# Kernel optimization log

Hardware: AMD Instinct MI355X
Metric: run time of the kernel (lower is better)

Reference implementation:

```python
import jax, jax.numpy as jnp
import numpy as np
from jax import lax

B, D = 512, 256
C = 10  # hidden conv channels


def setup_inputs() -> dict:
    key = jax.random.key(0)
    ks = jax.random.split(key, 9)
    x = jax.random.normal(ks[0], (B, D, D), jnp.float32)
    w1 = jax.random.normal(ks[1], (C, 1, 1, 1), jnp.float32) * 0.1   # Conv2d(1,10,1)
    b1 = jax.random.normal(ks[2], (C,), jnp.float32) * 0.01
    w2 = jax.random.normal(ks[3], (1, C, 3, 3), jnp.float32) * 0.05  # Conv2d(10,1,3,1,1)
    b2 = jax.random.normal(ks[4], (1,), jnp.float32) * 0.01
    fc1_w = jax.random.normal(ks[5], (4, D * B), jnp.float32) * (1.0 / np.sqrt(D * B))
    fc1_b = jax.random.normal(ks[6], (4,), jnp.float32) * 0.01
    fc2_w = jax.random.normal(ks[7], (2, 4), jnp.float32) * 0.5
    fc2_b = jax.random.normal(ks[8], (2,), jnp.float32) * 0.01
    return {"x": x, "w1": w1, "b1": b1, "w2": w2, "b2": b2,
            "fc1_w": fc1_w, "fc1_b": fc1_b, "fc2_w": fc2_w, "fc2_b": fc2_b}


def reference(x, w1, b1, w2, b2, fc1_w, fc1_b, fc2_w, fc2_b):
    # edge-to-edge: E[b,i,j] = row_sum(i) + col_sum(j)
    rs = x.sum(axis=-1)          # [B, D]
    cs = x.sum(axis=-2)          # [B, D]
    e = (rs[:, :, None] + cs[:, None, :])[:, None]  # [B, 1, D, D]
    # Conv2d(1, C, 1) == per-pixel scale+bias over channels
    h = jax.nn.relu(e * w1.reshape(1, C, 1, 1) + b1.reshape(1, C, 1, 1))  # [B, C, D, D]
    # convSym: lower-triangular mask each channel
    h = h * jnp.tril(jnp.ones((D, D), jnp.float32))
    # Conv2d(C, 1, 3, stride=1, pad=1)
    y = lax.conv_general_dilated(h, w2, (1, 1), 'SAME',
                                 dimension_numbers=('NCHW', 'OIHW', 'NCHW'))
    y = jax.nn.relu(y + b2.reshape(1, 1, 1, 1))[:, 0]  # [B, D, D]
    # edge-to-vertex: v[b,i] = row_sum + col_sum
    v = y.sum(axis=-1) + y.sum(axis=-2)  # [B, D]
    flat = v.reshape(-1)                  # [B*D]
    hfc = jax.nn.relu(fc1_w @ flat + fc1_b)
    return fc2_w @ hfc + fc2_b            # [2]
```

## Files before the change

kernel.cpp:

```cpp
#include <hip/hip_runtime.h>

#define DD 256
#define BB 512
#define NL 2048

#define OFF_RS   0
#define OFF_CSP  131072
#define OFF_HFC  655360
#define OFF_PAR  655368
#define OFF_TABP 655376
#define OFF_LUT  655648

typedef float v2f __attribute__((ext_vector_type(2)));

__device__ __forceinline__ v2f mk2(float a, float b) { v2f r; r.x = a; r.y = b; return r; }

__device__ __forceinline__ v2f fma2(v2f a, v2f b, v2f c) {
#if __has_builtin(__builtin_elementwise_fma)
  return __builtin_elementwise_fma(a, b, c);
#else
  return mk2(fmaf(a.x, b.x, c.x), fmaf(a.y, b.y, c.y));
#endif
}

__device__ __forceinline__ float wave_red(float v) {
#pragma unroll
  for (int off = 32; off > 0; off >>= 1) v += __shfl_down(v, off, 64);
  return v;
}

__global__ __launch_bounds__(256) void sum_kernel(const float* __restrict__ x,
                                                  const float* __restrict__ w1,
                                                  const float* __restrict__ b1,
                                                  const float* __restrict__ w2,
                                                  float* __restrict__ ws) {
  const int bq = blockIdx.x;
  const int tid = threadIdx.x;
  if (bq == 2048) {
    const int t = tid;
    float w1v[10], b1v[10], bp[10];
    int rank[10];
#pragma unroll
    for (int c = 0; c < 10; ++c) { w1v[c] = w1[c]; b1v[c] = b1[c]; bp[c] = -b1v[c] / w1v[c]; }
#pragma unroll
    for (int c = 0; c < 10; ++c) {
      int r = 0;
#pragma unroll
      for (int k = 0; k < 10; ++k)
        r += (bp[k] < bp[c] || (bp[k] == bp[c] && k < c)) ? 1 : 0;
      rank[c] = r;
    }
    float lo = bp[0], hi = bp[0];
#pragma unroll
    for (int c = 1; c < 10; ++c) { lo = fminf(lo, bp[c]); hi = fmaxf(hi, bp[c]); }
    const float step = (hi - lo) / (float)(NL - 3);
    if (t == 0) {
      ws[OFF_PAR]     = (float)(NL - 3) / (hi - lo);
      ws[OFF_PAR + 1] = 1.0f - lo * ((float)(NL - 3) / (hi - lo));
    }
    if (t < 99) {
      const int s = t / 9, tt = t % 9;
      const int dr = tt / 3, kc = tt % 3;
      float A = 0.f, Bv = 0.f;
      for (int c = 0; c < 10; ++c) {
        bool act = (w1v[c] > 0.f) ? (rank[c] < s)
                 : ((w1v[c] < 0.f) ? (rank[c] >= s) : (b1v[c] > 0.f));
        if (act) { A += w1v[c] * w2[c * 9 + tt]; Bv += b1v[c] * w2[c * 9 + tt]; }
      }
      const int base = (s * 3 + kc) * 8;
      const int posA = (dr == 2) ? 4 : dr;
      const int posB = (dr == 2) ? 5 : (2 + dr);
      ws[OFF_TABP + base + posA] = A;
      ws[OFF_TABP + base + posB] = Bv;
      ws[OFF_TABP + base + 6] = 0.f;
      ws[OFF_TABP + base + 7] = 0.f;
    }
    unsigned short* lut = (unsigned short*)(ws + OFF_LUT);
    for (int k = t; k < NL; k += 256) {
      const float xx = lo + (float)(k - 1) * step;
      int s = 0;
#pragma unroll
      for (int c = 0; c < 10; ++c) s += (bp[c] < xx) ? 1 : 0;
      lut[k] = (unsigned short)(s * 96);
    }
    return;
  }
  const int b = bq >> 2;
  const int q = bq & 3;
  const int lane = tid & 63;
  const int wv = tid >> 6;
  __shared__ float rowp[64][65];
  __shared__ float csl[4][DD];
  __shared__ float segp[4][64];
  float4 cacc = make_float4(0.f, 0.f, 0.f, 0.f);
  const float4* px = (const float4*)(x + ((size_t)b << 16) + ((size_t)(q * 64 + wv * 16) << 8));
#pragma unroll
  for (int r = 0; r < 16; ++r) {
    float4 val = px[r * 64 + lane];
    cacc.x += val.x; cacc.y += val.y; cacc.z += val.z; cacc.w += val.w;
    rowp[wv * 16 + r][lane] = (val.x + val.y) + (val.z + val.w);
  }
  ((float4*)csl[wv])[lane] = cacc;
  __syncthreads();
  {
    const int row = tid & 63, seg = tid >> 6;
    const float* rp = rowp[row] + seg * 16;
    float s = 0.f;
#pragma unroll
    for (int k = 0; k < 16; ++k) s += rp[k];
    segp[seg][row] = s;
  }
  __syncthreads();
  if (tid < 64)
    ws[OFF_RS + b * DD + q * 64 + tid] =
        (segp[0][tid] + segp[1][tid]) + (segp[2][tid] + segp[3][tid]);
  ws[OFF_CSP + bq * DD + tid] =
      (csl[0][tid] + csl[1][tid]) + (csl[2][tid] + csl[3][tid]);
  if (bq == 0 && tid < 4) ws[OFF_HFC + tid] = 0.f;
}

__global__ __launch_bounds__(1024, 8) void conv_kernel(const float* __restrict__ b2p,
                                                       const float* __restrict__ fc1w,
                                                       float* __restrict__ ws) {
  const int b = blockIdx.x;
  const int tid = threadIdx.x;
  const int w = tid >> 6;
  const int lane = tid & 63;
  const int seg = w >> 2;
  const int wb = (w - seg) & 3;
  const int j = wb * 64 + lane;
  const int jmin = wb * 64;
  const int r0 = seg * 64, r1 = r0 + 64;

  __shared__ __align__(16) float tabP[264];
  __shared__ float rs_s[DD];
  __shared__ float cs_s[DD];
  __shared__ __align__(16) float wkA[DD][4];
  __shared__ unsigned short lut_s[NL];
  __shared__ float segsum_s[4][4];
  __shared__ float red_s[64];

  ((unsigned int*)lut_s)[tid] = ((const unsigned int*)(ws + OFF_LUT))[tid];
  if (tid < 256) {
    rs_s[tid] = ws[OFF_RS + b * DD + tid];
  } else if (tid < 512) {
    const int t = tid - 256;
    const float* csp = ws + OFF_CSP + (b * 4) * DD + t;
    cs_s[t] = (csp[0] + csp[DD]) + (csp[2 * DD] + csp[3 * DD]);
  } else if (tid < 768) {
    const int r = tid - 512;
#pragma unroll
    for (int k = 0; k < 4; ++k) wkA[r][k] = fc1w[k * (BB * DD) + b * DD + r];
  } else {
    const int u = tid - 768;
    if (u < 256) tabP[u] = ws[OFF_TABP + u];
  }
  if (tid < 8) tabP[256 + tid] = ws[OFF_TABP + 256 + tid];
  __syncthreads();
  if (tid < 16) {
    const int ss = tid >> 2, k = tid & 3;
    float s = 0.f;
#pragma unroll
    for (int r = 0; r < 64; ++r) s += wkA[ss * 64 + r][k];
    segsum_s[ss][k] = s;
  }
  __syncthreads();

  const float inv_step = ws[OFF_PAR];
  const float bias = ws[OFF_PAR + 1];
  const float b2v = b2p[0];
  const float yb = fmaxf(b2v, 0.f);
  const float fxmax = (float)(NL - 1);

  float csr[3], vf[3];
  csr[0] = (j >= 1) ? cs_s[j - 1] : 0.f;
  csr[1] = cs_s[j];
  csr[2] = (j < DD - 1) ? cs_s[j + 1] : 0.f;
  vf[0] = (j >= 1) ? 1.f : 0.f;
  vf[1] = 1.f;
  vf[2] = (j < DD - 1) ? 1.f : 0.f;
  v2f vf2[3];
#pragma unroll
  for (int kc = 0; kc < 3; ++kc) vf2[kc] = mk2(vf[kc], vf[kc]);

  const int nt = min(max(jmin - 2 - r0, 0), 64);
  const int rfirst = r0 + nt;
  const int iend = (r1 == DD) ? DD - 1 : r1;

  float P = 0.f, Q = 0.f;
  float vcol = 64.f * yb;
  v2f a01 = mk2(yb * segsum_s[seg][0], yb * segsum_s[seg][1]);
  v2f a23 = mk2(yb * segsum_s[seg][2], yb * segsum_s[seg][3]);

#define TAP_CORE(KC, E, M2, MS)                                              \
  {                                                                          \
    float fx = fmaf((E), inv_step, bias);                                    \
    fx = fminf(fmaxf(fx, 0.f), fxmax);                                       \
    const int off = (int)lut_s[(int)fx];                                     \
    const char* tp = (const char*)tabP + (off + (KC) * 32);                  \
    const float4 ab = *(const float4*)tp;                   \
    const float2 ab2 = *(const float2*)(tp + 16);                 \
    v2f tv = fma2(mk2(ab.x, ab.y), mk2((E), (E)), mk2(ab.z, ab.w));          \
    R01 = fma2((M2), tv, R01);                                               \
    R2 = fmaf((MS), fmaf(ab2.x, (E), ab2.y), R2);                            \
  }

  if (rfirst < r1) {
    if (seg > wb) {
      for (int i = r0 - 1; i <= r0; ++i) {
        const float rsv = rs_s[i];
        v2f R01 = mk2(0.f, 0.f); float R2 = 0.f;
#pragma unroll
        for (int kc = 0; kc < 3; ++kc) {
          const float e = rsv + csr[kc];
          const float m = ((j - 1 + kc) <= i) ? vf[kc] : 0.f;
          TAP_CORE(kc, e, mk2(m, m), m)
        }
        P = Q + R01.y; Q = R01.x;
      }
      for (int i = r0 + 1; i <= iend; ++i) {
        const float rsv = rs_s[i];
        v2f R01 = mk2(0.f, 0.f); float R2 = 0.f;
#pragma unroll
        for (int kc = 0; kc < 3; ++kc) {
          const float e = rsv + csr[kc];
          TAP_CORE(kc, e, vf2[kc], vf[kc])
        }
        const float yd = fmaxf(P + R2 + b2v, 0.f) - yb;
        vcol += yd;
        const float4 wkv = *(const float4*)wkA[i - 1];
        a01 = fma2(mk2(yd, yd), mk2(wkv.x, wkv.y), a01);
        a23 = fma2(mk2(yd, yd), mk2(wkv.z, wkv.w), a23);
        P = Q + R01.y; Q = R01.x;
      }
    } else {
      const int ibeg = (nt > 0) ? rfirst - 1 : ((r0 == 0) ? 0 : r0 - 1);
      const int ffrom = rfirst + 1;
      for (int i = ibeg; i <= iend; ++i) {
        const float rsv = rs_s[i];
        v2f R01 = mk2(0.f, 0.f); float R2 = 0.f;
        if (j - 1 <= i) {
#pragma unroll
          for (int kc = 0; kc < 3; ++kc) {
            const float e = rsv + csr[kc];
            const float m = ((j - 1 + kc) <= i) ? vf[kc] : 0.f;
            TAP_CORE(kc, e, mk2(m, m), m)
          }
        }
        if (i >= ffrom) {
          const float yd = fmaxf(P + R2 + b2v, 0.f) - yb;
          vcol += yd;
          const float4 wkv = *(const float4*)wkA[i - 1];
          a01 = fma2(mk2(yd, yd), mk2(wkv.x, wkv.y), a01);
          a23 = fma2(mk2(yd, yd), mk2(wkv.z, wkv.w), a23);
        }
        P = Q + R01.y; Q = R01.x;
      }
    }
  }
  if (r1 == DD) {
    const float yd = fmaxf(P + b2v, 0.f) - yb;
    vcol += yd;
    const float4 wkv = *(const float4*)wkA[DD - 1];
    a01 = fma2(mk2(yd, yd), mk2(wkv.x, wkv.y), a01);
    a23 = fma2(mk2(yd, yd), mk2(wkv.z, wkv.w), a23);
  }

  const float4 wkj = *(const float4*)wkA[j];
  a01 = fma2(mk2(vcol, vcol), mk2(wkj.x, wkj.y), a01);
  a23 = fma2(mk2(vcol, vcol), mk2(wkj.z, wkj.w), a23);

  float acc0 = wave_red(a01.x), acc1 = wave_red(a01.y);
  float acc2 = wave_red(a23.x), acc3 = wave_red(a23.y);
  if (lane == 0) {
    red_s[w * 4 + 0] = acc0; red_s[w * 4 + 1] = acc1;
    red_s[w * 4 + 2] = acc2; red_s[w * 4 + 3] = acc3;
  }
  __syncthreads();
  if (tid < 4) {
    float s = 0.f;
#pragma unroll
    for (int wv = 0; wv < 16; ++wv) s += red_s[wv * 4 + tid];
    atomicAdd(&ws[OFF_HFC + tid], s);
  }
#undef TAP_CORE
}

__global__ void fc_kernel(const float* __restrict__ fc1b, const float* __restrict__ fc2w,
                          const float* __restrict__ fc2b, const float* __restrict__ ws,
                          float* __restrict__ out) {
  if (threadIdx.x == 0 && blockIdx.x == 0) {
    float o0 = fc2b[0], o1 = fc2b[1];
#pragma unroll
    for (int k = 0; k < 4; ++k) {
      float h = fmaxf(ws[OFF_HFC + k] + fc1b[k], 0.f);
      o0 += fc2w[k] * h;
      o1 += fc2w[4 + k] * h;
    }
    out[0] = o0; out[1] = o1;
  }
}

extern "C" void kernel_launch(void* const* d_in, const int* in_sizes, int n_in,
                              void* d_out, int out_size, void* d_ws, size_t ws_size,
                              hipStream_t stream) {
  const float* x    = (const float*)d_in[0];
  const float* w1   = (const float*)d_in[1];
  const float* b1   = (const float*)d_in[2];
  const float* w2   = (const float*)d_in[3];
  const float* b2   = (const float*)d_in[4];
  const float* fc1w = (const float*)d_in[5];
  const float* fc1b = (const float*)d_in[6];
  const float* fc2w = (const float*)d_in[7];
  const float* fc2b = (const float*)d_in[8];
  float* out = (float*)d_out;
  float* ws  = (float*)d_ws;

  hipLaunchKernelGGL(sum_kernel,  dim3(2049), dim3(256), 0, stream, x, w1, b1, w2, ws);
  hipLaunchKernelGGL(conv_kernel, dim3(512), dim3(1024), 0, stream, b2, fc1w, ws);
  hipLaunchKernelGGL(fc_kernel,   dim3(1), dim3(64), 0, stream, fc1b, fc2w, fc2b, ws, out);
}
```

Baseline: 243.2 us.

## Fuse row/column sum pass and table setup into the conv kernel

Merges the separate sum kernel into the conv kernel, so each 1024-thread block reads its own 256x256 slice of x, computes row and column sums in shared memory, and builds the LUT and convolution coefficient table locally instead of loading them from the workspace. This removes a kernel launch and the workspace round trip for the partial sums. The trade-off is that every block recomputes the small LUT and table, and the x read now happens inside a larger block with lower occupancy. Zeroing the fc accumulator is moved to a memset before the launch.

Measured after the change: 251.8 us. 3.6% more time.

```diff
diff --git a/kernel.cpp b/kernel.cpp
--- a/kernel.cpp
+++ b/kernel.cpp
@@ -4,12 +4,7 @@
 #define BB 512
 #define NL 2048
 
-#define OFF_RS   0
-#define OFF_CSP  131072
-#define OFF_HFC  655360
-#define OFF_PAR  655368
-#define OFF_TABP 655376
-#define OFF_LUT  655648
+#define OFF_HFC 0
 
 typedef float v2f __attribute__((ext_vector_type(2)));
 
@@ -29,145 +24,122 @@
   return v;
 }
 
-__global__ __launch_bounds__(256) void sum_kernel(const float* __restrict__ x,
-                                                  const float* __restrict__ w1,
-                                                  const float* __restrict__ b1,
-                                                  const float* __restrict__ w2,
-                                                  float* __restrict__ ws) {
-  const int bq = blockIdx.x;
-  const int tid = threadIdx.x;
-  if (bq == 2048) {
-    const int t = tid;
-    float w1v[10], b1v[10], bp[10];
-    int rank[10];
-#pragma unroll
-    for (int c = 0; c < 10; ++c) { w1v[c] = w1[c]; b1v[c] = b1[c]; bp[c] = -b1v[c] / w1v[c]; }
-#pragma unroll
-    for (int c = 0; c < 10; ++c) {
-      int r = 0;
-#pragma unroll
-      for (int k = 0; k < 10; ++k)
-        r += (bp[k] < bp[c] || (bp[k] == bp[c] && k < c)) ? 1 : 0;
-      rank[c] = r;
-    }
-    float lo = bp[0], hi = bp[0];
-#pragma unroll
-    for (int c = 1; c < 10; ++c) { lo = fminf(lo, bp[c]); hi = fmaxf(hi, bp[c]); }
-    const float step = (hi - lo) / (float)(NL - 3);
-    if (t == 0) {
-      ws[OFF_PAR]     = (float)(NL - 3) / (hi - lo);
-      ws[OFF_PAR + 1] = 1.0f - lo * ((float)(NL - 3) / (hi - lo));
-    }
-    if (t < 99) {
-      const int s = t / 9, tt = t % 9;
-      const int dr = tt / 3, kc = tt % 3;
-      float A = 0.f, Bv = 0.f;
-      for (int c = 0; c < 10; ++c) {
-        bool act = (w1v[c] > 0.f) ? (rank[c] < s)
-                 : ((w1v[c] < 0.f) ? (rank[c] >= s) : (b1v[c] > 0.f));
-        if (act) { A += w1v[c] * w2[c * 9 + tt]; Bv += b1v[c] * w2[c * 9 + tt]; }
-      }
-      const int base = (s * 3 + kc) * 8;
-      const int posA = (dr == 2) ? 4 : dr;
-      const int posB = (dr == 2) ? 5 : (2 + dr);
-      ws[OFF_TABP + base + posA] = A;
-      ws[OFF_TABP + base + posB] = Bv;
-      ws[OFF_TABP + base + 6] = 0.f;
-      ws[OFF_TABP + base + 7] = 0.f;
-    }
-    unsigned short* lut = (unsigned short*)(ws + OFF_LUT);
-    for (int k = t; k < NL; k += 256) {
-      const float xx = lo + (float)(k - 1) * step;
-      int s = 0;
-#pragma unroll
-      for (int c = 0; c < 10; ++c) s += (bp[c] < xx) ? 1 : 0;
-      lut[k] = (unsigned short)(s * 96);
-    }
-    return;
-  }
-  const int b = bq >> 2;
-  const int q = bq & 3;
-  const int lane = tid & 63;
-  const int wv = tid >> 6;
-  __shared__ float rowp[64][65];
-  __shared__ float csl[4][DD];
-  __shared__ float segp[4][64];
-  float4 cacc = make_float4(0.f, 0.f, 0.f, 0.f);
-  const float4* px = (const float4*)(x + ((size_t)b << 16) + ((size_t)(q * 64 + wv * 16) << 8));
-#pragma unroll
-  for (int r = 0; r < 16; ++r) {
-    float4 val = px[r * 64 + lane];
-    cacc.x += val.x; cacc.y += val.y; cacc.z += val.z; cacc.w += val.w;
-    rowp[wv * 16 + r][lane] = (val.x + val.y) + (val.z + val.w);
-  }
-  ((float4*)csl[wv])[lane] = cacc;
-  __syncthreads();
-  {
-    const int row = tid & 63, seg = tid >> 6;
-    const float* rp = rowp[row] + seg * 16;
-    float s = 0.f;
-#pragma unroll
-    for (int k = 0; k < 16; ++k) s += rp[k];
-    segp[seg][row] = s;
-  }
-  __syncthreads();
-  if (tid < 64)
-    ws[OFF_RS + b * DD + q * 64 + tid] =
-        (segp[0][tid] + segp[1][tid]) + (segp[2][tid] + segp[3][tid]);
-  ws[OFF_CSP + bq * DD + tid] =
-      (csl[0][tid] + csl[1][tid]) + (csl[2][tid] + csl[3][tid]);
-  if (bq == 0 && tid < 4) ws[OFF_HFC + tid] = 0.f;
-}
-
-__global__ __launch_bounds__(1024, 8) void conv_kernel(const float* __restrict__ b2p,
-                                                       const float* __restrict__ fc1w,
-                                                       float* __restrict__ ws) {
+__global__ __launch_bounds__(1024, 8) void fused_kernel(
+    const float* __restrict__ x,
+    const float* __restrict__ w1, const float* __restrict__ b1,
+    const float* __restrict__ w2, const float* __restrict__ b2p,
+    const float* __restrict__ fc1w, float* __restrict__ ws) {
   const int b = blockIdx.x;
   const int tid = threadIdx.x;
   const int w = tid >> 6;
   const int lane = tid & 63;
+
+  __shared__ float rowp[DD][17];
+  __shared__ float csl[16][DD];
+  __shared__ float rs_s[DD];
+  __shared__ float cs_s[DD];
+  __shared__ __align__(16) float tabP[264];
+  __shared__ __align__(16) float wkA[DD][4];
+  __shared__ unsigned short lut_s[NL];
+  __shared__ float segsum_s[4][4];
+  __shared__ float red_s[64];
+
+  float bp[10];
+  {
+#pragma unroll
+    for (int c = 0; c < 10; ++c) bp[c] = -b1[c] / w1[c];
+  }
+  float lo = bp[0], hi = bp[0];
+#pragma unroll
+  for (int c = 1; c < 10; ++c) { lo = fminf(lo, bp[c]); hi = fmaxf(hi, bp[c]); }
+  const float inv_step = (float)(NL - 3) / (hi - lo);
+  const float bias = 1.0f - lo * inv_step;
+  const float step = (hi - lo) / (float)(NL - 3);
+
+  {
+    float4 cacc = make_float4(0.f, 0.f, 0.f, 0.f);
+    const float4* px = (const float4*)(x + ((size_t)b << 16) + ((size_t)(w * 16) << 8));
+#pragma unroll
+    for (int r = 0; r < 16; ++r) {
+      float4 val = px[r * 64 + lane];
+      cacc.x += val.x; cacc.y += val.y; cacc.z += val.z; cacc.w += val.w;
+      float s = (val.x + val.y) + (val.z + val.w);
+      s += __shfl_xor(s, 32, 64);
+      s += __shfl_xor(s, 16, 64);
+      if (lane < 16) rowp[w * 16 + r][lane] = s;
+    }
+    ((float4*)csl[w])[lane] = cacc;
+  }
+
+  if (tid < 256) {
+#pragma unroll
+    for (int k = 0; k < 4; ++k) wkA[tid][k] = fc1w[k * (BB * DD) + b * DD + tid];
+  }
+  {
+    unsigned int pack = 0;
+#pragma unroll
+    for (int h = 0; h < 2; ++h) {
+      const int k = tid * 2 + h;
+      const float xx = lo + (float)(k - 1) * step;
+      int s = 0;
+#pragma unroll
+      for (int c = 0; c < 10; ++c) s += (bp[c] < xx) ? 1 : 0;
+      pack |= ((unsigned int)(s * 96)) << (16 * h);
+    }
+    ((unsigned int*)lut_s)[tid] = pack;
+  }
+  if (tid < 99) {
+    int rank[10];
+#pragma unroll
+    for (int c = 0; c < 10; ++c) {
+      int r = 0;
+#pragma unroll
+      for (int k = 0; k < 10; ++k)
+        r += (bp[k] < bp[c] || (bp[k] == bp[c] && k < c)) ? 1 : 0;
+      rank[c] = r;
+    }
+    const int s = tid / 9, tt = tid % 9;
+    const int dr = tt / 3, kc = tt % 3;
+    float A = 0.f, Bv = 0.f;
+    for (int c = 0; c < 10; ++c) {
+      const float w1c = w1[c], b1c = b1[c];
+      bool act = (w1c > 0.f) ? (rank[c] < s)
+               : ((w1c < 0.f) ? (rank[c] >= s) : (b1c > 0.f));
+      if (act) { A += w1c * w2[c * 9 + tt]; Bv += b1c * w2[c * 9 + tt]; }
+    }
+    const int base = (s * 3 + kc) * 8;
+    tabP[base + ((dr == 2) ? 4 : dr)]       = A;
+    tabP[base + ((dr == 2) ? 5 : (2 + dr))] = Bv;
+  }
+  __syncthreads();
+
+  if (tid < 256) {
+    const float* rp = rowp[tid];
+    float s = 0.f;
+#pragma unroll
+    for (int k = 0; k < 16; ++k) s += rp[k];
+    rs_s[tid] = s;
+  } else if (tid < 512) {
+    const int c = tid - 256;
+    float s = 0.f;
+#pragma unroll
+    for (int wv = 0; wv < 16; ++wv) s += csl[wv][c];
+    cs_s[c] = s;
+  } else if (tid < 528) {
+    const int ss = (tid - 512) >> 2, k = (tid - 512) & 3;
+    float s = 0.f;
+#pragma unroll
+    for (int r = 0; r < 64; ++r) s += wkA[ss * 64 + r][k];
+    segsum_s[ss][k] = s;
+  }
+  __syncthreads();
+
   const int seg = w >> 2;
   const int wb = (w - seg) & 3;
   const int j = wb * 64 + lane;
   const int jmin = wb * 64;
   const int r0 = seg * 64, r1 = r0 + 64;
 
-  __shared__ __align__(16) float tabP[264];
-  __shared__ float rs_s[DD];
-  __shared__ float cs_s[DD];
-  __shared__ __align__(16) float wkA[DD][4];
-  __shared__ unsigned short lut_s[NL];
-  __shared__ float segsum_s[4][4];
-  __shared__ float red_s[64];
-
-  ((unsigned int*)lut_s)[tid] = ((const unsigned int*)(ws + OFF_LUT))[tid];
-  if (tid < 256) {
-    rs_s[tid] = ws[OFF_RS + b * DD + tid];
-  } else if (tid < 512) {
-    const int t = tid - 256;
-    const float* csp = ws + OFF_CSP + (b * 4) * DD + t;
-    cs_s[t] = (csp[0] + csp[DD]) + (csp[2 * DD] + csp[3 * DD]);
-  } else if (tid < 768) {
-    const int r = tid - 512;
-#pragma unroll
-    for (int k = 0; k < 4; ++k) wkA[r][k] = fc1w[k * (BB * DD) + b * DD + r];
-  } else {
-    const int u = tid - 768;
-    if (u < 256) tabP[u] = ws[OFF_TABP + u];
-  }
-  if (tid < 8) tabP[256 + tid] = ws[OFF_TABP + 256 + tid];
-  __syncthreads();
-  if (tid < 16) {
-    const int ss = tid >> 2, k = tid & 3;
-    float s = 0.f;
-#pragma unroll
-    for (int r = 0; r < 64; ++r) s += wkA[ss * 64 + r][k];
-    segsum_s[ss][k] = s;
-  }
-  __syncthreads();
-
-  const float inv_step = ws[OFF_PAR];
-  const float bias = ws[OFF_PAR + 1];
   const float b2v = b2p[0];
   const float yb = fmaxf(b2v, 0.f);
   const float fxmax = (float)(NL - 1);
@@ -316,7 +288,8 @@
   float* out = (float*)d_out;
   float* ws  = (float*)d_ws;
 
-  hipLaunchKernelGGL(sum_kernel,  dim3(2049), dim3(256), 0, stream, x, w1, b1, w2, ws);
-  hipLaunchKernelGGL(conv_kernel, dim3(512), dim3(1024), 0, stream, b2, fc1w, ws);
-  hipLaunchKernelGGL(fc_kernel,   dim3(1), dim3(64), 0, stream, fc1b, fc2w, fc2b, ws, out);
-}
+  hipMemsetAsync(ws + OFF_HFC, 0, 4 * sizeof(float), stream);
+  hipLaunchKernelGGL(fused_kernel, dim3(512), dim3(1024), 0, stream,
+                     x, w1, b1, w2, b2, fc1w, ws);
+  hipLaunchKernelGGL(fc_kernel, dim3(1), dim3(64), 0, stream, fc1b, fc2w, fc2b, ws, out);
+}
```
